# Optimization experiments

Hardware: AMD Instinct MI355X
Metric: run time of the kernel (lower is better)

Reference implementation:

```python
import jax, jax.numpy as jnp
import numpy as np

N = 50000
E = 800000
H = 64
IN_NF = 8
EA = 2
N_LAYERS = 4
INNER = 7.0        # module.n_layers set to 7 when varDT=False (integration step count)
COORDS_WEIGHT = 1.0
EPS = 1e-8


def _mlp2(x, W1, b1, W2, b2, act_last=False):
    h = jax.nn.silu(x @ W1 + b1)
    h = h @ W2 + b2
    return jax.nn.silu(h) if act_last else h


def setup_inputs() -> dict:
    key = jax.random.key(0)
    ks = jax.random.split(key, 20)
    def g(k, shape, scale=None):
        s = scale if scale is not None else 1.0 / np.sqrt(shape[0])
        return (jax.random.normal(k, shape, jnp.float32) * s).astype(jnp.float32)
    return {
        "his": jax.random.normal(ks[0], (N, IN_NF), jnp.float32),
        "loc": jax.random.normal(ks[1], (N, 3), jnp.float32),
        "edges": jax.random.randint(ks[2], (2, E), 0, N),
        "vel": jax.random.normal(ks[3], (N, 3), jnp.float32),
        "edge_attr": jax.random.normal(ks[4], (E, EA), jnp.float32),
        "emb_W": g(ks[5], (IN_NF, H)), "emb_b": jnp.zeros((H,), jnp.float32),
        "e_W1": g(ks[6], (2 * H + 1 + EA, H)), "e_b1": jnp.zeros((H,), jnp.float32),
        "e_W2": g(ks[7], (H, H)), "e_b2": jnp.zeros((H,), jnp.float32),
        "c_W1": g(ks[8], (H, H)), "c_b1": jnp.zeros((H,), jnp.float32),
        "c_W2": g(ks[9], (H, 1), scale=1e-3),  # last coord layer: no bias, small init
        "v_W1": g(ks[10], (H, H)), "v_b1": jnp.zeros((H,), jnp.float32),
        "v_W2": g(ks[11], (H, 1)), "v_b2": jnp.zeros((1,), jnp.float32),
        "n_W1": g(ks[12], (2 * H, H)), "n_b1": jnp.zeros((H,), jnp.float32),
        "n_W2": g(ks[13], (H, H)), "n_b2": jnp.zeros((H,), jnp.float32),
    }


def _egcl(h, coord, vel, init_vel, row, col, edge_attr, p):
    # edge model: gather -> MLP
    coord_diff = coord[row] - coord[col]                         # [E,3]
    radial = jnp.sum(coord_diff * coord_diff, -1, keepdims=True)  # [E,1]
    e_in = jnp.concatenate([h[row], h[col], radial, edge_attr], -1)
    m = _mlp2(e_in, p["e_W1"], p["e_b1"], p["e_W2"], p["e_b2"], act_last=True)  # [E,H]
    # equivariant coordinate message + scatter-mean aggregation
    w = jax.nn.silu(m @ p["c_W1"] + p["c_b1"]) @ p["c_W2"]      # [E,1]
    trans = coord_diff * w                                       # [E,3]
    num = jax.ops.segment_sum(trans, row, num_segments=h.shape[0])
    cnt = jax.ops.segment_sum(jnp.ones((row.shape[0], 1), coord.dtype), row, num_segments=h.shape[0])
    acc = COORDS_WEIGHT * num / jnp.maximum(cnt, 1.0)            # [N,3]
    # second-order (velocity) update with learned gate + speed renorm (norm_vel=True)
    v_scale = _mlp2(h, p["v_W1"], p["v_b1"], p["v_W2"], p["v_b2"])  # [N,1]
    vel = v_scale * vel + acc / INNER
    speed0 = jnp.linalg.norm(init_vel, axis=-1, keepdims=True)
    vel = vel / (jnp.linalg.norm(vel, axis=-1, keepdims=True) + EPS) * speed0
    coord = coord + vel / INNER
    # node model: scatter-sum edge features + residual MLP (recurrent=True)
    agg_h = jax.ops.segment_sum(m, row, num_segments=h.shape[0])
    h_out = h + _mlp2(jnp.concatenate([h, agg_h], -1), p["n_W1"], p["n_b1"], p["n_W2"], p["n_b2"])
    return h_out, coord, vel


def reference(his, loc, edges, vel, edge_attr, emb_W, emb_b, e_W1, e_b1, e_W2, e_b2,
              c_W1, c_b1, c_W2, v_W1, v_b1, v_W2, v_b2, n_W1, n_b1, n_W2, n_b2):
    p = dict(e_W1=e_W1, e_b1=e_b1, e_W2=e_W2, e_b2=e_b2, c_W1=c_W1, c_b1=c_b1, c_W2=c_W2,
             v_W1=v_W1, v_b1=v_b1, v_W2=v_W2, v_b2=v_b2, n_W1=n_W1, n_b1=n_b1, n_W2=n_W2, n_b2=n_b2)
    row, col = edges[0], edges[1]
    his_e = his @ emb_W + emb_b                                  # embedding
    h1, x, v = _egcl(his_e, loc, vel, vel, row, col, edge_attr, p)
    h = his_e + h1
    for _ in range(1, N_LAYERS):                                 # shared-weight recurrent module
        hi, x, v = _egcl(h, x, v, vel, row, col, edge_attr, p)
        h = h + hi
    return (x, h, v)
```

## Files before the change

kernel.cpp:

```cpp
#include <hip/hip_runtime.h>
#include <hip/hip_bf16.h>
#include <stdint.h>

#define NN 50000
#define EE 800000
#define HD 64
#define AGS 72

typedef short short8 __attribute__((ext_vector_type(8)));
typedef float f32x4  __attribute__((ext_vector_type(4)));
typedef float f32x16 __attribute__((ext_vector_type(16)));
typedef uint  uint2v __attribute__((ext_vector_type(2)));

__device__ __forceinline__ float b2f(ushort u){ return __uint_as_float(((uint32_t)u)<<16); }
__device__ __forceinline__ ushort f2b(float f){
  uint32_t u = __float_as_uint(f);
  u += 0x7fffu + ((u>>16)&1u);
  return (ushort)(u>>16);
}
__device__ __forceinline__ uint pk2(float lo, float hi){
  union { __hip_bfloat162 b; uint u; } x;
  x.b = __float22bfloat162_rn(make_float2(lo, hi));
  return x.u;
}
__device__ __forceinline__ float silu_f(float x){
  return x * __builtin_amdgcn_rcpf(1.0f + __expf(-x));
}


__global__ __launch_bounds__(256) void k_count2(const int* __restrict__ erow,
    int* __restrict__ counts, const float* __restrict__ loc,
    const float* __restrict__ vel0, float4* __restrict__ coordw4,
    float4* __restrict__ velw4){
  int gid = blockIdx.x*256 + threadIdx.x;
  if (gid < EE) atomicAdd(&counts[erow[gid]], 1);
  if (gid < NN){
    float vx = vel0[gid*3+0], vy = vel0[gid*3+1], vz = vel0[gid*3+2];
    float sp = sqrtf(vx*vx + vy*vy + vz*vz);
    velw4[gid] = make_float4(vx, vy, vz, sp);
    coordw4[gid] = make_float4(loc[gid*3+0], loc[gid*3+1], loc[gid*3+2], 0.0f);
  }
}

__global__ __launch_bounds__(256) void k_bsum(const int* __restrict__ counts, int* __restrict__ bsum){
  __shared__ int sm[4];
  int tid = threadIdx.x;
  int i = blockIdx.x*256 + tid;
  int v = (i < NN) ? counts[i] : 0;
  #pragma unroll
  for (int off = 1; off < 64; off <<= 1) v += __shfl_xor(v, off);
  if ((tid & 63) == 0) sm[tid >> 6] = v;
  __syncthreads();
  if (tid == 0) bsum[blockIdx.x] = sm[0] + sm[1] + sm[2] + sm[3];
}

__global__ __launch_bounds__(256) void k_bscan(const int* __restrict__ bsum, int* __restrict__ bbase){
  __shared__ int sm[256];
  int tid = threadIdx.x;
  int v = (tid < 196) ? bsum[tid] : 0;
  sm[tid] = v;
  __syncthreads();
  #pragma unroll
  for (int off = 1; off < 256; off <<= 1){
    int t = (tid >= off) ? sm[tid - off] : 0;
    __syncthreads();
    sm[tid] += t;
    __syncthreads();
  }
  if (tid < 196) bbase[tid] = sm[tid] - v;
}

__global__ __launch_bounds__(256) void k_scatter(const int* __restrict__ counts,
    const int* __restrict__ bbase, int* __restrict__ cursor){
  __shared__ int sm[256];
  int tid = threadIdx.x;
  int i = blockIdx.x*256 + tid;
  int v = (i < NN) ? counts[i] : 0;
  sm[tid] = v;
  __syncthreads();
  #pragma unroll
  for (int off = 1; off < 256; off <<= 1){
    int t = (tid >= off) ? sm[tid - off] : 0;
    __syncthreads();
    sm[tid] += t;
    __syncthreads();
  }
  if (i < NN) cursor[i] = bbase[blockIdx.x] + sm[tid] - v;
}

__global__ __launch_bounds__(256) void k_fill(const int* __restrict__ erow,
    const int* __restrict__ ecol, const float* __restrict__ eattr,
    int* __restrict__ cursor, int4* __restrict__ erec){
  int e = blockIdx.x*256 + threadIdx.x;
  if (e < EE){
    int r = erow[e];
    int pos = atomicAdd(&cursor[r], 1);
    int4 rec;
    rec.x = r;
    rec.y = ecol[e];
    rec.z = __float_as_int(eattr[(size_t)e*2 + 0]);
    rec.w = __float_as_int(eattr[(size_t)e*2 + 1]);
    erec[pos] = rec;
  }
}

__global__ __launch_bounds__(256) void k_packall(const float* __restrict__ eW1,
    const float* __restrict__ b1, const float* __restrict__ eW2,
    const float* __restrict__ cW1, const float* __restrict__ nW1,
    const float* __restrict__ nW2, const float* __restrict__ vW1,
    ushort* __restrict__ dst){
  int idx = blockIdx.x*256 + threadIdx.x;
  if (idx >= 33792) return;
  float v;
  if (idx < 17408){
    int rel; const float* src; int isW1 = 0;
    if (idx < 9216){ rel = idx; src = eW1; isW1 = 1; }
    else if (idx < 13312){ rel = idx - 9216; src = eW2; }
    else { rel = idx - 13312; src = cW1; }
    int u = rel >> 9;
    int kt = u >> 1, mt = u & 1;
    int within = rel & 511;
    int lane = within >> 3, i = within & 7;
    int k = kt*16 + (lane>>5)*8 + i;
    int col = mt*32 + (lane & 31);
    if (isW1){
      if (k < 131) v = src[k*64 + col];
      else if (k == 131) v = b1[col];
      else v = 0.0f;
    } else {
      v = (k < 64) ? src[k*64 + col] : 0.0f;
    }
  } else {
    int rel = idx - 17408;
    const float* src; int kt; int Ksrc;
    if (rel < 8192){ src = nW1; kt = rel >> 11; Ksrc = 128; }
    else if (rel < 12288){ src = nW2; kt = (rel - 8192) >> 11; Ksrc = 64; }
    else { src = vW1; kt = (rel - 12288) >> 11; Ksrc = 64; }
    int within = rel & 2047;
    int i = within & 7;
    int lane = (within >> 3) & 63;
    int ct = (within >> 9) & 3;
    int k = kt*32 + (lane>>4)*8 + i;
    int col = ct*16 + (lane & 15);
    v = (k < Ksrc) ? src[k*64 + col] : 0.0f;
  }
  dst[idx] = f2b(v);
}

__global__ __launch_bounds__(256) void k_embed(const float* __restrict__ his,
    const float* __restrict__ embW, const float* __restrict__ embB,
    float* __restrict__ h, ushort* __restrict__ hb){
  int idx = blockIdx.x*256 + threadIdx.x;
  if (idx >= NN*HD) return;
  int n = idx >> 6, j = idx & 63;
  float s = embB[j];
  #pragma unroll
  for (int k = 0; k < 8; ++k) s += his[n*8 + k] * embW[k*64 + j];
  h[idx] = s;
  hb[idx] = f2b(s);
}

__global__ __launch_bounds__(256, 4) void k_edge(
    const ushort* __restrict__ hb, const float4* __restrict__ coord4,
    const int4* __restrict__ erec,
    const ushort* __restrict__ W1p, const ushort* __restrict__ W2p, const ushort* __restrict__ C1p,
    const float* __restrict__ b2, const float* __restrict__ cb1, const float* __restrict__ cw2,
    float* __restrict__ aggf)
{
  __shared__ __align__(16) uint XMT[128*38];
  __shared__ __align__(16) float TRL[128*4];
  const int tid = threadIdx.x;
  const int wave = tid >> 6, lane = tid & 63;
  const int e = lane & 31, h = lane >> 5;
  const int wt = wave * 32;
  const int slot = blockIdx.x*128 + wt + e;

  int4 er = erec[slot];
  const int rA = er.x, cA = er.y;

  float4 crd = coord4[rA], ccd = coord4[cA];
  float dx = crd.x-ccd.x, dy = crd.y-ccd.y, dz = crd.z-ccd.z;
  float radial = dx*dx + dy*dy + dz*dz;

  const short8* W1f = reinterpret_cast<const short8*>(W1p);
  const short8* W2f = reinterpret_cast<const short8*>(W2p);
  const short8* C1f = reinterpret_cast<const short8*>(C1p);
  const int wrow = (wt + e)*38;

  {
    short8 bf[9];
    #pragma unroll
    for (int kt = 0; kt < 4; ++kt)
      bf[kt] = *reinterpret_cast<const short8*>(hb + (size_t)rA*HD + kt*16 + h*8);
    #pragma unroll
    for (int kt = 0; kt < 4; ++kt)
      bf[4+kt] = *reinterpret_cast<const short8*>(hb + (size_t)cA*HD + kt*16 + h*8);
    short8 t8 = {0,0,0,0,0,0,0,0};
    if (h == 0){
      t8[0] = (short)f2b(radial);
      t8[1] = (short)f2b(__int_as_float(er.z));
      t8[2] = (short)f2b(__int_as_float(er.w));
      t8[3] = (short)0x3F80;
    }
    bf[8] = t8;

    #pragma unroll 1
    for (int mt = 0; mt < 2; ++mt){
      f32x16 a;
      #pragma unroll
      for (int r = 0; r < 16; ++r) a[r] = 0.0f;
      #pragma unroll
      for (int kt = 0; kt < 9; ++kt)
        a = __builtin_amdgcn_mfma_f32_32x32x16_bf16(W1f[(kt*2+mt)*64 + lane], bf[kt], a, 0,0,0);
      #pragma unroll
      for (int q = 0; q < 4; ++q){
        uint u0 = pk2(silu_f(a[4*q+0]), silu_f(a[4*q+1]));
        uint u1 = pk2(silu_f(a[4*q+2]), silu_f(a[4*q+3]));
        *reinterpret_cast<uint2v*>(&XMT[wrow + mt*16 + q*4 + h*2]) = (uint2v){u0, u1};
      }
    }
  }
  __builtin_amdgcn_sched_barrier(0);

  {
    short8 xf[4];
    #pragma unroll
    for (int kt = 0; kt < 4; ++kt)
      xf[kt] = *reinterpret_cast<const short8*>(&XMT[wrow + kt*8 + h*4]);
    #pragma unroll 1
    for (int mt = 0; mt < 2; ++mt){
      f32x16 a;
      #pragma unroll
      for (int q = 0; q < 4; ++q){
        f32x4 bq = *reinterpret_cast<const f32x4*>(b2 + mt*32 + q*8 + h*4);
        #pragma unroll
        for (int r = 0; r < 4; ++r) a[4*q+r] = bq[r];
      }
      #pragma unroll
      for (int kt = 0; kt < 4; ++kt)
        a = __builtin_amdgcn_mfma_f32_32x32x16_bf16(W2f[(kt*2+mt)*64 + lane], xf[kt], a, 0,0,0);
      #pragma unroll
      for (int q = 0; q < 4; ++q){
        uint u0 = pk2(silu_f(a[4*q+0]), silu_f(a[4*q+1]));
        uint u1 = pk2(silu_f(a[4*q+2]), silu_f(a[4*q+3]));
        *reinterpret_cast<uint2v*>(&XMT[wrow + mt*16 + q*4 + h*2]) = (uint2v){u0, u1};
      }
    }
  }
  __builtin_amdgcn_sched_barrier(0);

  float pw = 0.0f;
  {
    short8 xg[4];
    #pragma unroll
    for (int kt = 0; kt < 4; ++kt)
      xg[kt] = *reinterpret_cast<const short8*>(&XMT[wrow + kt*8 + h*4]);
    #pragma unroll 1
    for (int mt = 0; mt < 2; ++mt){
      f32x16 a;
      #pragma unroll
      for (int q = 0; q < 4; ++q){
        f32x4 bq = *reinterpret_cast<const f32x4*>(cb1 + mt*32 + q*8 + h*4);
        #pragma unroll
        for (int r = 0; r < 4; ++r) a[4*q+r] = bq[r];
      }
      #pragma unroll
      for (int kt = 0; kt < 4; ++kt)
        a = __builtin_amdgcn_mfma_f32_32x32x16_bf16(C1f[(kt*2+mt)*64 + lane], xg[kt], a, 0,0,0);
      #pragma unroll
      for (int q = 0; q < 4; ++q){
        f32x4 cwq = *reinterpret_cast<const f32x4*>(cw2 + mt*32 + q*8 + h*4);
        #pragma unroll
        for (int r = 0; r < 4; ++r) pw += silu_f(a[4*q+r]) * cwq[r];
      }
    }
  }
  pw += __shfl_xor(pw, 32);
  if (h == 0){
    f32x4 t = {dx*pw, dy*pw, dz*pw, 0.0f};
    *reinterpret_cast<f32x4*>(&TRL[(wt + e)*4]) = t;
  }
  __builtin_amdgcn_sched_barrier(0);

  const ushort* mvals = reinterpret_cast<const ushort*>(XMT);
  float sum = 0.f, ts = 0.f;
  int rcur = __builtin_amdgcn_readlane(rA, 0);
  #pragma unroll
  for (int i = 0; i < 32; ++i){
    sum += b2f(mvals[(wt + i)*76 + lane]);
    if (lane < 3) ts += TRL[(wt + i)*4 + lane];
    int rnext = (i < 31) ? __builtin_amdgcn_readlane(rA, i+1) : -1;
    if (rnext != rcur){
      atomicAdd(&aggf[(size_t)rcur*AGS + lane], sum);
      if (lane < 3) atomicAdd(&aggf[(size_t)rcur*AGS + 64 + lane], ts);
      sum = 0.f; ts = 0.f; rcur = rnext;
    }
  }
}

__global__ __launch_bounds__(256) void k_node(
    const ushort* __restrict__ hb, float* __restrict__ aggf, const float* __restrict__ h_in,
    const ushort* __restrict__ nW1p, const ushort* __restrict__ nW2p, const ushort* __restrict__ vW1p,
    const float* __restrict__ nb1, const float* __restrict__ nb2,
    const float* __restrict__ vb1, const float* __restrict__ vW2, const float* __restrict__ vb2,
    const int* __restrict__ counts, float4* __restrict__ velw4, float4* __restrict__ coordw4,
    float* __restrict__ h_out, ushort* __restrict__ hb_out,
    float* __restrict__ xout, float* __restrict__ vout, int last)
{
  __shared__ __align__(16) ushort HID[64*88];
  __shared__ float VS[64];
  const int tid = threadIdx.x;
  const int wave = tid >> 6, lane = tid & 63;
  const int c = lane & 15, g = lane >> 4;
  const int wt = wave * 16;
  const int nbase = blockIdx.x * 64;
  int nA = nbase + wt + c;
  int nAc = (nA < NN) ? nA : (NN-1);

  short8 af[4];
  af[0] = *reinterpret_cast<const short8*>(hb + (size_t)nAc*HD + g*8);
  af[1] = *reinterpret_cast<const short8*>(hb + (size_t)nAc*HD + 32 + g*8);
  {
    const float* ag = aggf + (size_t)nAc*AGS;
    f32x4 q0 = *reinterpret_cast<const f32x4*>(ag + g*8);
    f32x4 q1 = *reinterpret_cast<const f32x4*>(ag + g*8 + 4);
    f32x4 q2 = *reinterpret_cast<const f32x4*>(ag + 32 + g*8);
    f32x4 q3 = *reinterpret_cast<const f32x4*>(ag + 32 + g*8 + 4);
    union FB { ushort u[8]; short8 s; };
    FB f2_, f3_;
    #pragma unroll
    for (int i = 0; i < 4; ++i){ f2_.u[i] = f2b(q0[i]); f2_.u[4+i] = f2b(q1[i]); }
    #pragma unroll
    for (int i = 0; i < 4; ++i){ f3_.u[i] = f2b(q2[i]); f3_.u[4+i] = f2b(q3[i]); }
    af[2] = f2_.s;
    af[3] = f3_.s;
  }
  const short8* N1f = reinterpret_cast<const short8*>(nW1p);
  const short8* N2f = reinterpret_cast<const short8*>(nW2p);
  const short8* V1f = reinterpret_cast<const short8*>(vW1p);

  f32x4 acc[4];
  #pragma unroll
  for (int ct = 0; ct < 4; ++ct){
    float bb = nb1[ct*16 + c];
    acc[ct] = (f32x4){bb,bb,bb,bb};
  }
  #pragma unroll
  for (int kt = 0; kt < 4; ++kt){
    #pragma unroll
    for (int ct = 0; ct < 4; ++ct){
      acc[ct] = __builtin_amdgcn_mfma_f32_16x16x32_bf16(af[kt], N1f[(kt*4+ct)*64 + lane], acc[ct], 0,0,0);
    }
  }
  #pragma unroll
  for (int ct = 0; ct < 4; ++ct){
    int col = ct*16 + c;
    #pragma unroll
    for (int r = 0; r < 4; ++r){
      HID[(wt + g*4 + r)*88 + col] = f2b(silu_f(acc[ct][r]));
    }
  }

  f32x4 av[4];
  #pragma unroll
  for (int ct = 0; ct < 4; ++ct){
    float bb = vb1[ct*16 + c];
    av[ct] = (f32x4){bb,bb,bb,bb};
  }
  #pragma unroll
  for (int kt = 0; kt < 2; ++kt){
    #pragma unroll
    for (int ct = 0; ct < 4; ++ct){
      av[ct] = __builtin_amdgcn_mfma_f32_16x16x32_bf16(af[kt], V1f[(kt*4+ct)*64 + lane], av[ct], 0,0,0);
    }
  }
  float pw[4] = {0.f,0.f,0.f,0.f};
  #pragma unroll
  for (int ct = 0; ct < 4; ++ct){
    float vw = vW2[ct*16 + c];
    #pragma unroll
    for (int r = 0; r < 4; ++r) pw[r] += silu_f(av[ct][r]) * vw;
  }
  #pragma unroll
  for (int off = 1; off < 16; off <<= 1){
    #pragma unroll
    for (int r = 0; r < 4; ++r) pw[r] += __shfl_xor(pw[r], off, 16);
  }
  if (c == 0){
    float vbias = vb2[0];
    #pragma unroll
    for (int r = 0; r < 4; ++r) VS[wt + g*4 + r] = pw[r] + vbias;
  }

  short8 h0 = *reinterpret_cast<const short8*>(&HID[(wt + c)*88 + g*8]);
  short8 h1 = *reinterpret_cast<const short8*>(&HID[(wt + c)*88 + 32 + g*8]);
  f32x4 a2[4];
  #pragma unroll
  for (int ct = 0; ct < 4; ++ct){
    float bb = nb2[ct*16 + c];
    a2[ct] = (f32x4){bb,bb,bb,bb};
  }
  #pragma unroll
  for (int ct = 0; ct < 4; ++ct)
    a2[ct] = __builtin_amdgcn_mfma_f32_16x16x32_bf16(h0, N2f[(0*4+ct)*64 + lane], a2[ct], 0,0,0);
  #pragma unroll
  for (int ct = 0; ct < 4; ++ct)
    a2[ct] = __builtin_amdgcn_mfma_f32_16x16x32_bf16(h1, N2f[(1*4+ct)*64 + lane], a2[ct], 0,0,0);
  #pragma unroll
  for (int ct = 0; ct < 4; ++ct){
    int col = ct*16 + c;
    #pragma unroll
    for (int r = 0; r < 4; ++r){
      int n = nbase + wt + g*4 + r;
      if (n < NN){
        size_t off = (size_t)n*HD + col;
        float v = 2.0f*h_in[off] + a2[ct][r];
        h_out[off] = v;
        hb_out[off] = f2b(v);
      }
    }
  }

  __syncthreads();
  if (tid < 64){
    int n = nbase + tid;
    if (n < NN){
      float vsn = VS[tid];
      float inv = 1.0f / fmaxf((float)counts[n], 1.0f);
      const float* ag = aggf + (size_t)n*AGS + 64;
      float ax = ag[0]*inv, ay = ag[1]*inv, az = ag[2]*inv;
      float4 vv = velw4[n];
      float4 cc = coordw4[n];
      float v0 = vsn*vv.x + ax*(1.0f/7.0f);
      float v1 = vsn*vv.y + ay*(1.0f/7.0f);
      float v2 = vsn*vv.z + az*(1.0f/7.0f);
      float s = vv.w / (sqrtf(v0*v0 + v1*v1 + v2*v2) + 1e-8f);
      v0 *= s; v1 *= s; v2 *= s;
      float c0 = cc.x + v0*(1.0f/7.0f);
      float c1 = cc.y + v1*(1.0f/7.0f);
      float c2 = cc.z + v2*(1.0f/7.0f);
      if (last){
        vout[n*3+0] = v0; vout[n*3+1] = v1; vout[n*3+2] = v2;
        xout[n*3+0] = c0; xout[n*3+1] = c1; xout[n*3+2] = c2;
      } else {
        velw4[n] = make_float4(v0, v1, v2, vv.w);
        coordw4[n] = make_float4(c0, c1, c2, 0.0f);
      }
    }
  }

  __syncthreads();
  int nvalid = NN - nbase; if (nvalid > 64) nvalid = 64;
  float* zb = aggf + (size_t)nbase*AGS;
  for (int idx2 = tid; idx2 < nvalid*AGS; idx2 += 256) zb[idx2] = 0.0f;
}

extern "C" void kernel_launch(void* const* d_in, const int* in_sizes, int n_in,
                              void* d_out, int out_size, void* d_ws, size_t ws_size,
                              hipStream_t stream)
{
  const float* his  = (const float*)d_in[0];
  const float* loc  = (const float*)d_in[1];
  const int*   edges= (const int*)d_in[2];
  const float* vel0 = (const float*)d_in[3];
  const float* eatt = (const float*)d_in[4];
  const float* embW = (const float*)d_in[5];
  const float* embB = (const float*)d_in[6];
  const float* eW1  = (const float*)d_in[7];
  const float* eB1  = (const float*)d_in[8];
  const float* eW2  = (const float*)d_in[9];
  const float* eB2  = (const float*)d_in[10];
  const float* cW1  = (const float*)d_in[11];
  const float* cB1  = (const float*)d_in[12];
  const float* cW2  = (const float*)d_in[13];
  const float* vW1  = (const float*)d_in[14];
  const float* vB1  = (const float*)d_in[15];
  const float* vW2  = (const float*)d_in[16];
  const float* vB2  = (const float*)d_in[17];
  const float* nW1  = (const float*)d_in[18];
  const float* nB1  = (const float*)d_in[19];
  const float* nW2  = (const float*)d_in[20];
  const float* nB2  = (const float*)d_in[21];
  const int* erow = edges;
  const int* ecol = edges + EE;

  char* ws = (char*)d_ws;
  size_t off = 0;
  auto alloc = [&](size_t bytes)->char*{
    char* p = ws + off;
    off = (off + bytes + 255) & ~(size_t)255;
    return p;
  };
  ushort* hb     = (ushort*)alloc((size_t)NN*HD*2);
  int*    counts = (int*)   alloc((size_t)NN*4);
  int*    cursor = (int*)   alloc((size_t)NN*4);
  int*    bsum   = (int*)   alloc(256*4);
  int*    bbase  = (int*)   alloc(256*4);
  float4* coordw4= (float4*)alloc((size_t)NN*16);
  float4* velw4  = (float4*)alloc((size_t)NN*16);
  float*  aggf   = (float*) alloc((size_t)NN*AGS*4);
  ushort* allp   = (ushort*)alloc(33792*2);
  int4*   erec   = (int4*)  alloc((size_t)EE*16);

  ushort* eW1p32 = allp;
  ushort* eW2p32 = allp + 9216;
  ushort* cW1p32 = allp + 13312;
  ushort* nW1p   = allp + 17408;
  ushort* nW2p   = allp + 25600;
  ushort* vW1p   = allp + 29696;

  float* xout = (float*)d_out;
  float* hout = (float*)d_out + (size_t)NN*3;
  float* vout = (float*)d_out + (size_t)NN*3 + (size_t)NN*HD;

  hipMemsetAsync(counts, 0, (size_t)NN*4, stream);
  hipMemsetAsync(aggf, 0, (size_t)NN*AGS*4, stream);
  k_count2<<<3125,256,0,stream>>>(erow, counts, loc, vel0, coordw4, velw4);
  k_bsum<<<196,256,0,stream>>>(counts, bsum);
  k_bscan<<<1,256,0,stream>>>(bsum, bbase);
  k_scatter<<<196,256,0,stream>>>(counts, bbase, cursor);
  k_fill<<<3125,256,0,stream>>>(erow, ecol, eatt, cursor, erec);
  k_packall<<<132,256,0,stream>>>(eW1, eB1, eW2, cW1, nW1, nW2, vW1, allp);
  k_embed<<<12500,256,0,stream>>>(his, embW, embB, hout, hb);

  for (int L = 0; L < 4; ++L){
    k_edge<<<6250,256,0,stream>>>(hb, coordw4, erec,
        eW1p32, eW2p32, cW1p32, eB2, cB1, cW2, aggf);
    k_node<<<782,256,0,stream>>>(hb, aggf, hout, nW1p, nW2p, vW1p,
        nB1, nB2, vB1, vW2, vB2, counts, velw4, coordw4,
        hout, hb, xout, vout, (L==3) ? 1 : 0);
  }
}
```

Baseline: 513.5 us.

## Keep edge MLP activations in registers between MFMA stages via permuted weight packing

Permutes the K ordering of the packed W2 and C1 weights so that the accumulator output layout of one 32x32x16 MFMA can be reused directly as the B operand of the next. The edge kernel then passes SiLU outputs between the three MLP stages in registers instead of round-tripping through LDS. LDS is written once, for the final message, with a permuted layout and a matching lane offset in the scatter loop. This removes LDS stores and loads plus scheduling barriers, at the cost of more live registers and more intricate index mapping.

```diff
diff --git a/kernel.cpp b/kernel.cpp
--- a/kernel.cpp
+++ b/kernel.cpp
@@ -121,14 +121,15 @@
     int kt = u >> 1, mt = u & 1;
     int within = rel & 511;
     int lane = within >> 3, i = within & 7;
-    int k = kt*16 + (lane>>5)*8 + i;
     int col = mt*32 + (lane & 31);
     if (isW1){
+      int k = kt*16 + (lane>>5)*8 + i;
       if (k < 131) v = src[k*64 + col];
       else if (k == 131) v = b1[col];
       else v = 0.0f;
     } else {
-      v = (k < 64) ? src[k*64 + col] : 0.0f;
+      int k = 32*(kt>>1) + 16*(kt&1) + 8*(i>>2) + 2*((i>>1)&1) + (i&1) + 4*(lane>>5);
+      v = src[k*64 + col];
     }
   } else {
     int rel = idx - 17408;
@@ -167,7 +168,7 @@
     const float* __restrict__ b2, const float* __restrict__ cb1, const float* __restrict__ cw2,
     float* __restrict__ aggf)
 {
-  __shared__ __align__(16) uint XMT[128*38];
+  __shared__ __align__(16) uint XMT[128*34];
   __shared__ __align__(16) float TRL[128*4];
   const int tid = threadIdx.x;
   const int wave = tid >> 6, lane = tid & 63;
@@ -185,8 +186,10 @@
   const short8* W1f = reinterpret_cast<const short8*>(W1p);
   const short8* W2f = reinterpret_cast<const short8*>(W2p);
   const short8* C1f = reinterpret_cast<const short8*>(C1p);
-  const int wrow = (wt + e)*38;
-
+
+  union U4 { uint u[4]; short8 s; };
+
+  uint uw[16];
   {
     short8 bf[9];
     #pragma unroll
@@ -213,66 +216,56 @@
       for (int kt = 0; kt < 9; ++kt)
         a = __builtin_amdgcn_mfma_f32_32x32x16_bf16(W1f[(kt*2+mt)*64 + lane], bf[kt], a, 0,0,0);
       #pragma unroll
-      for (int q = 0; q < 4; ++q){
-        uint u0 = pk2(silu_f(a[4*q+0]), silu_f(a[4*q+1]));
-        uint u1 = pk2(silu_f(a[4*q+2]), silu_f(a[4*q+3]));
-        *reinterpret_cast<uint2v*>(&XMT[wrow + mt*16 + q*4 + h*2]) = (uint2v){u0, u1};
-      }
-    }
-  }
-  __builtin_amdgcn_sched_barrier(0);
-
-  {
-    short8 xf[4];
-    #pragma unroll
-    for (int kt = 0; kt < 4; ++kt)
-      xf[kt] = *reinterpret_cast<const short8*>(&XMT[wrow + kt*8 + h*4]);
-    #pragma unroll 1
-    for (int mt = 0; mt < 2; ++mt){
-      f32x16 a;
+      for (int s = 0; s < 8; ++s)
+        uw[mt*8 + s] = pk2(silu_f(a[2*s]), silu_f(a[2*s+1]));
+    }
+  }
+
+  uint uw2[16];
+  #pragma unroll 1
+  for (int mt = 0; mt < 2; ++mt){
+    f32x16 a;
+    #pragma unroll
+    for (int q = 0; q < 4; ++q){
+      f32x4 bq = *reinterpret_cast<const f32x4*>(b2 + mt*32 + q*8 + h*4);
       #pragma unroll
-      for (int q = 0; q < 4; ++q){
-        f32x4 bq = *reinterpret_cast<const f32x4*>(b2 + mt*32 + q*8 + h*4);
-        #pragma unroll
-        for (int r = 0; r < 4; ++r) a[4*q+r] = bq[r];
-      }
+      for (int r = 0; r < 4; ++r) a[4*q+r] = bq[r];
+    }
+    #pragma unroll
+    for (int kt = 0; kt < 4; ++kt){
+      U4 t; t.u[0]=uw[kt*4+0]; t.u[1]=uw[kt*4+1]; t.u[2]=uw[kt*4+2]; t.u[3]=uw[kt*4+3];
+      a = __builtin_amdgcn_mfma_f32_32x32x16_bf16(W2f[(kt*2+mt)*64 + lane], t.s, a, 0,0,0);
+    }
+    #pragma unroll
+    for (int s = 0; s < 8; ++s)
+      uw2[mt*8 + s] = pk2(silu_f(a[2*s]), silu_f(a[2*s+1]));
+  }
+
+  const int wrow = (wt + e)*34 + h*16;
+  #pragma unroll
+  for (int t = 0; t < 8; ++t)
+    *reinterpret_cast<uint2v*>(&XMT[wrow + 2*t]) = (uint2v){uw2[2*t], uw2[2*t+1]};
+
+  float pw = 0.0f;
+  #pragma unroll 1
+  for (int mt = 0; mt < 2; ++mt){
+    f32x16 a;
+    #pragma unroll
+    for (int q = 0; q < 4; ++q){
+      f32x4 bq = *reinterpret_cast<const f32x4*>(cb1 + mt*32 + q*8 + h*4);
       #pragma unroll
-      for (int kt = 0; kt < 4; ++kt)
-        a = __builtin_amdgcn_mfma_f32_32x32x16_bf16(W2f[(kt*2+mt)*64 + lane], xf[kt], a, 0,0,0);
+      for (int r = 0; r < 4; ++r) a[4*q+r] = bq[r];
+    }
+    #pragma unroll
+    for (int kt = 0; kt < 4; ++kt){
+      U4 t; t.u[0]=uw2[kt*4+0]; t.u[1]=uw2[kt*4+1]; t.u[2]=uw2[kt*4+2]; t.u[3]=uw2[kt*4+3];
+      a = __builtin_amdgcn_mfma_f32_32x32x16_bf16(C1f[(kt*2+mt)*64 + lane], t.s, a, 0,0,0);
+    }
+    #pragma unroll
+    for (int q = 0; q < 4; ++q){
+      f32x4 cwq = *reinterpret_cast<const f32x4*>(cw2 + mt*32 + q*8 + h*4);
       #pragma unroll
-      for (int q = 0; q < 4; ++q){
-        uint u0 = pk2(silu_f(a[4*q+0]), silu_f(a[4*q+1]));
-        uint u1 = pk2(silu_f(a[4*q+2]), silu_f(a[4*q+3]));
-        *reinterpret_cast<uint2v*>(&XMT[wrow + mt*16 + q*4 + h*2]) = (uint2v){u0, u1};
-      }
-    }
-  }
-  __builtin_amdgcn_sched_barrier(0);
-
-  float pw = 0.0f;
-  {
-    short8 xg[4];
-    #pragma unroll
-    for (int kt = 0; kt < 4; ++kt)
-      xg[kt] = *reinterpret_cast<const short8*>(&XMT[wrow + kt*8 + h*4]);
-    #pragma unroll 1
-    for (int mt = 0; mt < 2; ++mt){
-      f32x16 a;
-      #pragma unroll
-      for (int q = 0; q < 4; ++q){
-        f32x4 bq = *reinterpret_cast<const f32x4*>(cb1 + mt*32 + q*8 + h*4);
-        #pragma unroll
-        for (int r = 0; r < 4; ++r) a[4*q+r] = bq[r];
-      }
-      #pragma unroll
-      for (int kt = 0; kt < 4; ++kt)
-        a = __builtin_amdgcn_mfma_f32_32x32x16_bf16(C1f[(kt*2+mt)*64 + lane], xg[kt], a, 0,0,0);
-      #pragma unroll
-      for (int q = 0; q < 4; ++q){
-        f32x4 cwq = *reinterpret_cast<const f32x4*>(cw2 + mt*32 + q*8 + h*4);
-        #pragma unroll
-        for (int r = 0; r < 4; ++r) pw += silu_f(a[4*q+r]) * cwq[r];
-      }
+      for (int r = 0; r < 4; ++r) pw += silu_f(a[4*q+r]) * cwq[r];
     }
   }
   pw += __shfl_xor(pw, 32);
@@ -280,14 +273,15 @@
     f32x4 t = {dx*pw, dy*pw, dz*pw, 0.0f};
     *reinterpret_cast<f32x4*>(&TRL[(wt + e)*4]) = t;
   }
-  __builtin_amdgcn_sched_barrier(0);
-
+
+  const int j = lane;
+  const int soff = (((j>>5)*8 + ((j>>3)&3)*2 + ((j>>1)&1)) + ((j>>2)&1)*16)*2 + (j&1);
   const ushort* mvals = reinterpret_cast<const ushort*>(XMT);
   float sum = 0.f, ts = 0.f;
   int rcur = __builtin_amdgcn_readlane(rA, 0);
   #pragma unroll
   for (int i = 0; i < 32; ++i){
-    sum += b2f(mvals[(wt + i)*76 + lane]);
+    sum += b2f(mvals[(wt + i)*68 + soff]);
     if (lane < 3) ts += TRL[(wt + i)*4 + lane];
     int rnext = (i < 31) ? __builtin_amdgcn_readlane(rA, i+1) : -1;
     if (rnext != rcur){
```

Measured after the change: 551.8 us. 7.5% more time.

## Process two edge tiles per block with prefetched gathers and XCD-aware block swizzle

Applied to the files above, without the earlier changes.

Each k_edge block now handles 256 edges in two 128-edge tiles instead of one, and the grid is halved. The second tile's node-feature and coordinate gathers are issued during the first tile's coordinate-MLP stage, so their memory latency is meant to overlap with MFMA work. Block indices are also remapped so that each XCD processes a contiguous range of sorted edges, which should improve L2 locality for the gathers and atomics. The cost is higher register pressure from holding the second tile's operands, which may reduce occupancy under the launch bounds of 4 blocks per CU.

```diff
diff --git a/kernel.cpp b/kernel.cpp
--- a/kernel.cpp
+++ b/kernel.cpp
@@ -173,45 +173,66 @@
   const int wave = tid >> 6, lane = tid & 63;
   const int e = lane & 31, h = lane >> 5;
   const int wt = wave * 32;
-  const int slot = blockIdx.x*128 + wt + e;
-
-  int4 er = erec[slot];
-  const int rA = er.x, cA = er.y;
-
-  float4 crd = coord4[rA], ccd = coord4[cA];
-  float dx = crd.x-ccd.x, dy = crd.y-ccd.y, dz = crd.z-ccd.z;
-  float radial = dx*dx + dy*dy + dz*dz;
+
+  const int bid = blockIdx.x;
+  const int xcd = bid & 7, bx = bid >> 3;
+  const int swz = (xcd < 5) ? (xcd*391 + bx) : (5*391 + (xcd-5)*390 + bx);
+  const int base = swz * 256;
+
+  const int slot0 = base + wt + e;
+  const int slot1 = base + 128 + wt + e;
+  int4 er0 = erec[slot0];
+  int4 er1 = erec[slot1];
+  const int rA0 = er0.x, cA0 = er0.y;
+  const int rA1 = er1.x, cA1 = er1.y;
 
   const short8* W1f = reinterpret_cast<const short8*>(W1p);
   const short8* W2f = reinterpret_cast<const short8*>(W2p);
   const short8* C1f = reinterpret_cast<const short8*>(C1p);
-  const int wrow = (wt + e)*38;
-
+
+  short8 bfa0,bfa1,bfa2,bfa3,bfa4,bfa5,bfa6,bfa7,bfa8;
+  bfa0 = *reinterpret_cast<const short8*>(hb + (size_t)rA0*HD +  0 + h*8);
+  bfa1 = *reinterpret_cast<const short8*>(hb + (size_t)rA0*HD + 16 + h*8);
+  bfa2 = *reinterpret_cast<const short8*>(hb + (size_t)rA0*HD + 32 + h*8);
+  bfa3 = *reinterpret_cast<const short8*>(hb + (size_t)rA0*HD + 48 + h*8);
+  bfa4 = *reinterpret_cast<const short8*>(hb + (size_t)cA0*HD +  0 + h*8);
+  bfa5 = *reinterpret_cast<const short8*>(hb + (size_t)cA0*HD + 16 + h*8);
+  bfa6 = *reinterpret_cast<const short8*>(hb + (size_t)cA0*HD + 32 + h*8);
+  bfa7 = *reinterpret_cast<const short8*>(hb + (size_t)cA0*HD + 48 + h*8);
+  float4 crd0 = coord4[rA0], ccd0 = coord4[cA0];
+  float dx0 = crd0.x-ccd0.x, dy0 = crd0.y-ccd0.y, dz0 = crd0.z-ccd0.z;
   {
-    short8 bf[9];
-    #pragma unroll
-    for (int kt = 0; kt < 4; ++kt)
-      bf[kt] = *reinterpret_cast<const short8*>(hb + (size_t)rA*HD + kt*16 + h*8);
-    #pragma unroll
-    for (int kt = 0; kt < 4; ++kt)
-      bf[4+kt] = *reinterpret_cast<const short8*>(hb + (size_t)cA*HD + kt*16 + h*8);
+    float radial = dx0*dx0 + dy0*dy0 + dz0*dz0;
     short8 t8 = {0,0,0,0,0,0,0,0};
     if (h == 0){
       t8[0] = (short)f2b(radial);
-      t8[1] = (short)f2b(__int_as_float(er.z));
-      t8[2] = (short)f2b(__int_as_float(er.w));
+      t8[1] = (short)f2b(__int_as_float(er0.z));
+      t8[2] = (short)f2b(__int_as_float(er0.w));
       t8[3] = (short)0x3F80;
     }
-    bf[8] = t8;
-
+    bfa8 = t8;
+  }
+
+  const int wrow = (wt + e)*38;
+  const ushort* mvals = reinterpret_cast<const ushort*>(XMT);
+  short8 bfb0,bfb1,bfb2,bfb3,bfb4,bfb5,bfb6,bfb7,bfb8;
+  float dx1, dy1, dz1;
+
+  {
     #pragma unroll 1
     for (int mt = 0; mt < 2; ++mt){
       f32x16 a;
       #pragma unroll
       for (int r = 0; r < 16; ++r) a[r] = 0.0f;
-      #pragma unroll
-      for (int kt = 0; kt < 9; ++kt)
-        a = __builtin_amdgcn_mfma_f32_32x32x16_bf16(W1f[(kt*2+mt)*64 + lane], bf[kt], a, 0,0,0);
+      a = __builtin_amdgcn_mfma_f32_32x32x16_bf16(W1f[(0*2+mt)*64 + lane], bfa0, a, 0,0,0);
+      a = __builtin_amdgcn_mfma_f32_32x32x16_bf16(W1f[(1*2+mt)*64 + lane], bfa1, a, 0,0,0);
+      a = __builtin_amdgcn_mfma_f32_32x32x16_bf16(W1f[(2*2+mt)*64 + lane], bfa2, a, 0,0,0);
+      a = __builtin_amdgcn_mfma_f32_32x32x16_bf16(W1f[(3*2+mt)*64 + lane], bfa3, a, 0,0,0);
+      a = __builtin_amdgcn_mfma_f32_32x32x16_bf16(W1f[(4*2+mt)*64 + lane], bfa4, a, 0,0,0);
+      a = __builtin_amdgcn_mfma_f32_32x32x16_bf16(W1f[(5*2+mt)*64 + lane], bfa5, a, 0,0,0);
+      a = __builtin_amdgcn_mfma_f32_32x32x16_bf16(W1f[(6*2+mt)*64 + lane], bfa6, a, 0,0,0);
+      a = __builtin_amdgcn_mfma_f32_32x32x16_bf16(W1f[(7*2+mt)*64 + lane], bfa7, a, 0,0,0);
+      a = __builtin_amdgcn_mfma_f32_32x32x16_bf16(W1f[(8*2+mt)*64 + lane], bfa8, a, 0,0,0);
       #pragma unroll
       for (int q = 0; q < 4; ++q){
         uint u0 = pk2(silu_f(a[4*q+0]), silu_f(a[4*q+1]));
@@ -219,14 +240,12 @@
         *reinterpret_cast<uint2v*>(&XMT[wrow + mt*16 + q*4 + h*2]) = (uint2v){u0, u1};
       }
     }
-  }
-  __builtin_amdgcn_sched_barrier(0);
-
-  {
-    short8 xf[4];
-    #pragma unroll
-    for (int kt = 0; kt < 4; ++kt)
-      xf[kt] = *reinterpret_cast<const short8*>(&XMT[wrow + kt*8 + h*4]);
+    __builtin_amdgcn_sched_barrier(0);
+    short8 xf0 = *reinterpret_cast<const short8*>(&XMT[wrow +  0 + h*4]);
+    short8 xf1 = *reinterpret_cast<const short8*>(&XMT[wrow +  8 + h*4]);
+    short8 xf2 = *reinterpret_cast<const short8*>(&XMT[wrow + 16 + h*4]);
+    short8 xf3 = *reinterpret_cast<const short8*>(&XMT[wrow + 24 + h*4]);
+
     #pragma unroll 1
     for (int mt = 0; mt < 2; ++mt){
       f32x16 a;
@@ -236,9 +255,10 @@
         #pragma unroll
         for (int r = 0; r < 4; ++r) a[4*q+r] = bq[r];
       }
-      #pragma unroll
-      for (int kt = 0; kt < 4; ++kt)
-        a = __builtin_amdgcn_mfma_f32_32x32x16_bf16(W2f[(kt*2+mt)*64 + lane], xf[kt], a, 0,0,0);
+      a = __builtin_amdgcn_mfma_f32_32x32x16_bf16(W2f[(0*2+mt)*64 + lane], xf0, a, 0,0,0);
+      a = __builtin_amdgcn_mfma_f32_32x32x16_bf16(W2f[(1*2+mt)*64 + lane], xf1, a, 0,0,0);
+      a = __builtin_amdgcn_mfma_f32_32x32x16_bf16(W2f[(2*2+mt)*64 + lane], xf2, a, 0,0,0);
+      a = __builtin_amdgcn_mfma_f32_32x32x16_bf16(W2f[(3*2+mt)*64 + lane], xf3, a, 0,0,0);
       #pragma unroll
       for (int q = 0; q < 4; ++q){
         uint u0 = pk2(silu_f(a[4*q+0]), silu_f(a[4*q+1]));
@@ -246,15 +266,35 @@
         *reinterpret_cast<uint2v*>(&XMT[wrow + mt*16 + q*4 + h*2]) = (uint2v){u0, u1};
       }
     }
-  }
-  __builtin_amdgcn_sched_barrier(0);
-
-  float pw = 0.0f;
-  {
-    short8 xg[4];
-    #pragma unroll
-    for (int kt = 0; kt < 4; ++kt)
-      xg[kt] = *reinterpret_cast<const short8*>(&XMT[wrow + kt*8 + h*4]);
+    __builtin_amdgcn_sched_barrier(0);
+    short8 xg0 = *reinterpret_cast<const short8*>(&XMT[wrow +  0 + h*4]);
+    short8 xg1 = *reinterpret_cast<const short8*>(&XMT[wrow +  8 + h*4]);
+    short8 xg2 = *reinterpret_cast<const short8*>(&XMT[wrow + 16 + h*4]);
+    short8 xg3 = *reinterpret_cast<const short8*>(&XMT[wrow + 24 + h*4]);
+
+    bfb0 = *reinterpret_cast<const short8*>(hb + (size_t)rA1*HD +  0 + h*8);
+    bfb1 = *reinterpret_cast<const short8*>(hb + (size_t)rA1*HD + 16 + h*8);
+    bfb2 = *reinterpret_cast<const short8*>(hb + (size_t)rA1*HD + 32 + h*8);
+    bfb3 = *reinterpret_cast<const short8*>(hb + (size_t)rA1*HD + 48 + h*8);
+    bfb4 = *reinterpret_cast<const short8*>(hb + (size_t)cA1*HD +  0 + h*8);
+    bfb5 = *reinterpret_cast<const short8*>(hb + (size_t)cA1*HD + 16 + h*8);
+    bfb6 = *reinterpret_cast<const short8*>(hb + (size_t)cA1*HD + 32 + h*8);
+    bfb7 = *reinterpret_cast<const short8*>(hb + (size_t)cA1*HD + 48 + h*8);
+    {
+      float4 crd1 = coord4[rA1], ccd1 = coord4[cA1];
+      dx1 = crd1.x-ccd1.x; dy1 = crd1.y-ccd1.y; dz1 = crd1.z-ccd1.z;
+      float radial = dx1*dx1 + dy1*dy1 + dz1*dz1;
+      short8 t8 = {0,0,0,0,0,0,0,0};
+      if (h == 0){
+        t8[0] = (short)f2b(radial);
+        t8[1] = (short)f2b(__int_as_float(er1.z));
+        t8[2] = (short)f2b(__int_as_float(er1.w));
+        t8[3] = (short)0x3F80;
+      }
+      bfb8 = t8;
+    }
+
+    float pw = 0.0f;
     #pragma unroll 1
     for (int mt = 0; mt < 2; ++mt){
       f32x16 a;
@@ -264,9 +304,10 @@
         #pragma unroll
         for (int r = 0; r < 4; ++r) a[4*q+r] = bq[r];
       }
-      #pragma unroll
-      for (int kt = 0; kt < 4; ++kt)
-        a = __builtin_amdgcn_mfma_f32_32x32x16_bf16(C1f[(kt*2+mt)*64 + lane], xg[kt], a, 0,0,0);
+      a = __builtin_amdgcn_mfma_f32_32x32x16_bf16(C1f[(0*2+mt)*64 + lane], xg0, a, 0,0,0);
+      a = __builtin_amdgcn_mfma_f32_32x32x16_bf16(C1f[(1*2+mt)*64 + lane], xg1, a, 0,0,0);
+      a = __builtin_amdgcn_mfma_f32_32x32x16_bf16(C1f[(2*2+mt)*64 + lane], xg2, a, 0,0,0);
+      a = __builtin_amdgcn_mfma_f32_32x32x16_bf16(C1f[(3*2+mt)*64 + lane], xg3, a, 0,0,0);
       #pragma unroll
       for (int q = 0; q < 4; ++q){
         f32x4 cwq = *reinterpret_cast<const f32x4*>(cw2 + mt*32 + q*8 + h*4);
@@ -274,26 +315,122 @@
         for (int r = 0; r < 4; ++r) pw += silu_f(a[4*q+r]) * cwq[r];
       }
     }
-  }
-  pw += __shfl_xor(pw, 32);
-  if (h == 0){
-    f32x4 t = {dx*pw, dy*pw, dz*pw, 0.0f};
-    *reinterpret_cast<f32x4*>(&TRL[(wt + e)*4]) = t;
-  }
-  __builtin_amdgcn_sched_barrier(0);
-
-  const ushort* mvals = reinterpret_cast<const ushort*>(XMT);
-  float sum = 0.f, ts = 0.f;
-  int rcur = __builtin_amdgcn_readlane(rA, 0);
-  #pragma unroll
-  for (int i = 0; i < 32; ++i){
-    sum += b2f(mvals[(wt + i)*76 + lane]);
-    if (lane < 3) ts += TRL[(wt + i)*4 + lane];
-    int rnext = (i < 31) ? __builtin_amdgcn_readlane(rA, i+1) : -1;
-    if (rnext != rcur){
-      atomicAdd(&aggf[(size_t)rcur*AGS + lane], sum);
-      if (lane < 3) atomicAdd(&aggf[(size_t)rcur*AGS + 64 + lane], ts);
-      sum = 0.f; ts = 0.f; rcur = rnext;
+    pw += __shfl_xor(pw, 32);
+    if (h == 0){
+      f32x4 t = {dx0*pw, dy0*pw, dz0*pw, 0.0f};
+      *reinterpret_cast<f32x4*>(&TRL[(wt + e)*4]) = t;
+    }
+    __builtin_amdgcn_sched_barrier(0);
+
+    float sum = 0.f, ts = 0.f;
+    int rcur = __builtin_amdgcn_readlane(rA0, 0);
+    #pragma unroll
+    for (int i = 0; i < 32; ++i){
+      sum += b2f(mvals[(wt + i)*76 + lane]);
+      if (lane < 3) ts += TRL[(wt + i)*4 + lane];
+      int rnext = (i < 31) ? __builtin_amdgcn_readlane(rA0, i+1) : -1;
+      if (rnext != rcur){
+        atomicAdd(&aggf[(size_t)rcur*AGS + lane], sum);
+        if (lane < 3) atomicAdd(&aggf[(size_t)rcur*AGS + 64 + lane], ts);
+        sum = 0.f; ts = 0.f; rcur = rnext;
+      }
+    }
+  }
+
+  {
+    #pragma unroll 1
+    for (int mt = 0; mt < 2; ++mt){
+      f32x16 a;
+      #pragma unroll
+      for (int r = 0; r < 16; ++r) a[r] = 0.0f;
+      a = __builtin_amdgcn_mfma_f32_32x32x16_bf16(W1f[(0*2+mt)*64 + lane], bfb0, a, 0,0,0);
+      a = __builtin_amdgcn_mfma_f32_32x32x16_bf16(W1f[(1*2+mt)*64 + lane], bfb1, a, 0,0,0);
+      a = __builtin_amdgcn_mfma_f32_32x32x16_bf16(W1f[(2*2+mt)*64 + lane], bfb2, a, 0,0,0);
+      a = __builtin_amdgcn_mfma_f32_32x32x16_bf16(W1f[(3*2+mt)*64 + lane], bfb3, a, 0,0,0);
+      a = __builtin_amdgcn_mfma_f32_32x32x16_bf16(W1f[(4*2+mt)*64 + lane], bfb4, a, 0,0,0);
+      a = __builtin_amdgcn_mfma_f32_32x32x16_bf16(W1f[(5*2+mt)*64 + lane], bfb5, a, 0,0,0);
+      a = __builtin_amdgcn_mfma_f32_32x32x16_bf16(W1f[(6*2+mt)*64 + lane], bfb6, a, 0,0,0);
+      a = __builtin_amdgcn_mfma_f32_32x32x16_bf16(W1f[(7*2+mt)*64 + lane], bfb7, a, 0,0,0);
+      a = __builtin_amdgcn_mfma_f32_32x32x16_bf16(W1f[(8*2+mt)*64 + lane], bfb8, a, 0,0,0);
+      #pragma unroll
+      for (int q = 0; q < 4; ++q){
+        uint u0 = pk2(silu_f(a[4*q+0]), silu_f(a[4*q+1]));
+        uint u1 = pk2(silu_f(a[4*q+2]), silu_f(a[4*q+3]));
+        *reinterpret_cast<uint2v*>(&XMT[wrow + mt*16 + q*4 + h*2]) = (uint2v){u0, u1};
+      }
+    }
+    __builtin_amdgcn_sched_barrier(0);
+    short8 xf0 = *reinterpret_cast<const short8*>(&XMT[wrow +  0 + h*4]);
+    short8 xf1 = *reinterpret_cast<const short8*>(&XMT[wrow +  8 + h*4]);
+    short8 xf2 = *reinterpret_cast<const short8*>(&XMT[wrow + 16 + h*4]);
+    short8 xf3 = *reinterpret_cast<const short8*>(&XMT[wrow + 24 + h*4]);
+
+    #pragma unroll 1
+    for (int mt = 0; mt < 2; ++mt){
+      f32x16 a;
+      #pragma unroll
+      for (int q = 0; q < 4; ++q){
+        f32x4 bq = *reinterpret_cast<const f32x4*>(b2 + mt*32 + q*8 + h*4);
+        #pragma unroll
+        for (int r = 0; r < 4; ++r) a[4*q+r] = bq[r];
+      }
+      a = __builtin_amdgcn_mfma_f32_32x32x16_bf16(W2f[(0*2+mt)*64 + lane], xf0, a, 0,0,0);
+      a = __builtin_amdgcn_mfma_f32_32x32x16_bf16(W2f[(1*2+mt)*64 + lane], xf1, a, 0,0,0);
+      a = __builtin_amdgcn_mfma_f32_32x32x16_bf16(W2f[(2*2+mt)*64 + lane], xf2, a, 0,0,0);
+      a = __builtin_amdgcn_mfma_f32_32x32x16_bf16(W2f[(3*2+mt)*64 + lane], xf3, a, 0,0,0);
+      #pragma unroll
+      for (int q = 0; q < 4; ++q){
+        uint u0 = pk2(silu_f(a[4*q+0]), silu_f(a[4*q+1]));
+        uint u1 = pk2(silu_f(a[4*q+2]), silu_f(a[4*q+3]));
+        *reinterpret_cast<uint2v*>(&XMT[wrow + mt*16 + q*4 + h*2]) = (uint2v){u0, u1};
+      }
+    }
+    __builtin_amdgcn_sched_barrier(0);
+    short8 xg0 = *reinterpret_cast<const short8*>(&XMT[wrow +  0 + h*4]);
+    short8 xg1 = *reinterpret_cast<const short8*>(&XMT[wrow +  8 + h*4]);
+    short8 xg2 = *reinterpret_cast<const short8*>(&XMT[wrow + 16 + h*4]);
+    short8 xg3 = *reinterpret_cast<const short8*>(&XMT[wrow + 24 + h*4]);
+
+    float pw = 0.0f;
+    #pragma unroll 1
+    for (int mt = 0; mt < 2; ++mt){
+      f32x16 a;
+      #pragma unroll
+      for (int q = 0; q < 4; ++q){
+        f32x4 bq = *reinterpret_cast<const f32x4*>(cb1 + mt*32 + q*8 + h*4);
+        #pragma unroll
+        for (int r = 0; r < 4; ++r) a[4*q+r] = bq[r];
+      }
+      a = __builtin_amdgcn_mfma_f32_32x32x16_bf16(C1f[(0*2+mt)*64 + lane], xg0, a, 0,0,0);
+      a = __builtin_amdgcn_mfma_f32_32x32x16_bf16(C1f[(1*2+mt)*64 + lane], xg1, a, 0,0,0);
+      a = __builtin_amdgcn_mfma_f32_32x32x16_bf16(C1f[(2*2+mt)*64 + lane], xg2, a, 0,0,0);
+      a = __builtin_amdgcn_mfma_f32_32x32x16_bf16(C1f[(3*2+mt)*64 + lane], xg3, a, 0,0,0);
+      #pragma unroll
+      for (int q = 0; q < 4; ++q){
+        f32x4 cwq = *reinterpret_cast<const f32x4*>(cw2 + mt*32 + q*8 + h*4);
+        #pragma unroll
+        for (int r = 0; r < 4; ++r) pw += silu_f(a[4*q+r]) * cwq[r];
+      }
+    }
+    pw += __shfl_xor(pw, 32);
+    if (h == 0){
+      f32x4 t = {dx1*pw, dy1*pw, dz1*pw, 0.0f};
+      *reinterpret_cast<f32x4*>(&TRL[(wt + e)*4]) = t;
+    }
+    __builtin_amdgcn_sched_barrier(0);
+
+    float sum = 0.f, ts = 0.f;
+    int rcur = __builtin_amdgcn_readlane(rA1, 0);
+    #pragma unroll
+    for (int i = 0; i < 32; ++i){
+      sum += b2f(mvals[(wt + i)*76 + lane]);
+      if (lane < 3) ts += TRL[(wt + i)*4 + lane];
+      int rnext = (i < 31) ? __builtin_amdgcn_readlane(rA1, i+1) : -1;
+      if (rnext != rcur){
+        atomicAdd(&aggf[(size_t)rcur*AGS + lane], sum);
+        if (lane < 3) atomicAdd(&aggf[(size_t)rcur*AGS + 64 + lane], ts);
+        sum = 0.f; ts = 0.f; rcur = rnext;
+      }
     }
   }
 }
@@ -524,7 +661,7 @@
   k_embed<<<12500,256,0,stream>>>(his, embW, embB, hout, hb);
 
   for (int L = 0; L < 4; ++L){
-    k_edge<<<6250,256,0,stream>>>(hb, coordw4, erec,
+    k_edge<<<3125,256,0,stream>>>(hb, coordw4, erec,
         eW1p32, eW2p32, cW1p32, eB2, cB1, cW2, aggf);
     k_node<<<782,256,0,stream>>>(hb, aggf, hout, nW1p, nW2p, vW1p,
         nB1, nB2, vB1, vW2, vB2, counts, velw4, coordw4,
```

New measurement: 594.5 us. +15.8%, slower.
